# Kernel optimization log

Measured on AMD Instinct MI355X. Metric: run time of the kernel, lower is better.

Reference implementation:

```python
import jax, jax.numpy as jnp
import numpy as np

H = 2048
MAX_DEPTH = 2
BASIS = 4


def setup_inputs() -> dict:
    key = jax.random.key(0)
    ks = jax.random.split(key, 16)
    s = 0.02

    def w(k, shape):
        return jax.random.normal(k, shape, dtype=jnp.float32) * s

    return dict(
        x=jax.random.normal(ks[0], (1, H), dtype=jnp.float32),
        h=jax.random.normal(ks[1], (1, H), dtype=jnp.float32),
        c=jax.random.normal(ks[2], (1, H), dtype=jnp.float32),
        Wq=w(ks[3], (H, H)), Wk=w(ks[4], (H, H)), Wv=w(ks[5], (H, H)), Wo=w(ks[6], (H, H)),
        Wih=w(ks[7], (H, 4 * H)), Whh=w(ks[8], (H, 4 * H)),
        b_lstm=jnp.zeros((4 * H,), jnp.float32),
        router_w=w(ks[9], (H, BASIS)), router_b=jnp.zeros((BASIS,), jnp.float32),
        expert_w=w(ks[10], (BASIS, H, H)), expert_b=jnp.zeros((BASIS, H), jnp.float32),
        dr_w=w(ks[11], (H, MAX_DEPTH + 1)),
        # bias the depth router toward the deepest choice so the recursion tree is exercised
        dr_b=jnp.array([0.0, 1.0, 5.0], jnp.float32),
        ram_w=w(ks[12], (2 * H, H)), ram_b=jnp.zeros((H,), jnp.float32),
        ag_w=w(ks[13], (2 * H, H)), ag_b=jnp.zeros((H,), jnp.float32),
    )


def reference(x, h, c, Wq, Wk, Wv, Wo, Wih, Whh, b_lstm, router_w, router_b,
              expert_w, expert_b, dr_w, dr_b, ram_w, ram_b, ag_w, ag_b):
    def cell_step(x_, h_, c_):
        # Single-token multi-head attention: softmax over a length-1 axis is
        # identically 1, so attention collapses to (h @ Wv) @ Wo; Wq/Wk are
        # parameters with zero effective gradient (matches torch behavior).
        attn = (h_ @ Wv) @ Wo
        gates = x_ @ Wih + attn @ Whh + b_lstm  # [1, 4H]
        i, f, g, o = jnp.split(gates, 4, axis=1)
        c2 = jax.nn.sigmoid(f) * c_ + jax.nn.sigmoid(i) * jnp.tanh(g)
        h2 = jax.nn.sigmoid(o) * jnp.tanh(c2)
        return h2, h2, c2

    def path_gate(hh):
        p = jax.nn.softmax(hh @ router_w + router_b, axis=1)          # [1, E]
        eo = jnp.einsum('bh,ehk->bek', hh, expert_w) + expert_b        # [1, E, H]
        return jnp.einsum('be,bek->bk', p, eo)                         # [1, H]

    def ramanujan(states):
        # alternating-harmonic (Ramanujan-summation style) weighted reduction
        agg = states[0] * 0.0
        for n, s in enumerate(states):
            agg = agg + (((-1.0) ** n) / (n + 1)) * s
        return jnp.concatenate([agg, states[0]], axis=1) @ ram_w + ram_b

    def fwd(x_, h_, c_, depth):
        so, hs, cs = cell_step(x_, h_, c_)
        hp = path_gate(hs)
        # mirrors torch.no_grad() + .item() host sync
        chosen = int(jnp.argmax(hp @ dr_w + dr_b, axis=1)[0])
        steps = min(chosen, max(0, MAX_DEPTH - depth))
        if steps <= 0:
            return so, hp, cs
        h_cur, c_cur, final = hp, cs, so
        states = [h_cur]
        for _ in range(steps):
            damping = 1.0 / (depth + 1) ** 2
            ro, hnr, cn = fwd(x_, h_cur, c_cur, depth + 1)
            h_next = h_cur + damping * (hnr - h_cur)  # torch.lerp
            states.append(h_next)
            h_cur, c_cur, final = h_next, cn, ro
        anchor = ramanujan(states)
        g = jax.nn.sigmoid(jnp.concatenate([h_cur, anchor], axis=1) @ ag_w + ag_b)
        return final, g * anchor + (1.0 - g) * h_cur, c_cur

    return fwd(x, h, c, 0)
```

## Files before the change

kernel.cpp:

```cpp
#include <hip/hip_runtime.h>
#include <math.h>


#define H 2048
#define NB 512
#define PREP_NB 2048
typedef unsigned short u16;
typedef float f4v __attribute__((ext_vector_type(4)));

struct P {
  const float *x, *h0, *c0, *Wv, *Wo, *Wih, *Whh, *b_lstm, *router_w, *router_b,
              *expert_w, *expert_b, *dr_w, *dr_b, *ram_w, *ram_b, *ag_w, *ag_b;
  const u16 *bWv, *bWo, *bWhh, *bEx;
  float* out;
  float* ws;
};

constexpr int CTRU   = 8192;
constexpr int DL     = 8192;
constexpr int GT     = 8208;
constexpr int NODE   = 16400;
constexpr int NODESZ = 26624;
constexpr int THV = 0, ATT = 2048, GAC = 4096, EO = 12288, SO = 20480, CS = 22528, HP = 24576;
constexpr int FIN    = NODE + 5 * NODESZ;
constexpr int FINSZ  = 8192;
constexpr int ANC = 0, GCC = 2048, HNo = 4096, AGGo = 6144;
constexpr int RH1 = FIN + 3 * FINSZ;
constexpr int RF1 = RH1 + 2048;
constexpr int RC1 = RH1 + 4096;
constexpr int ZTOT = 5 * 20480 + 3 * 4096;
constexpr size_t BF_BYTE_OFF = 786432;
constexpr size_t oWo  = 4194304;
constexpr size_t oWhh = 8388608;
constexpr size_t oEx  = 25165824;
constexpr size_t BF_TOT = 41943040;

__device__ __forceinline__ float sigm(float v) { return 1.f / (1.f + expf(-v)); }

__device__ __forceinline__ float coh_f(const float* p) {
  return __hip_atomic_load(p, __ATOMIC_RELAXED, __HIP_MEMORY_SCOPE_AGENT);
}
__device__ __forceinline__ void coh_st(float* p, float v) {
  __hip_atomic_store(p, v, __ATOMIC_RELAXED, __HIP_MEMORY_SCOPE_AGENT);
}

__device__ __forceinline__ float bfl(unsigned u) { union { unsigned x; float f; } c; c.x = u << 16; return c.f; }
__device__ __forceinline__ float bfh(unsigned u) { union { unsigned x; float f; } c; c.x = u & 0xFFFF0000u; return c.f; }
__device__ __forceinline__ u16 f2bf(float f) {
  unsigned u = __float_as_uint(f);
  u += 0x7FFFu + ((u >> 16) & 1u);
  return (u16)(u >> 16);
}

template <typename WT> struct W4;
template <> struct W4<float> {
  static __device__ __forceinline__ void load(const float* p, float* w) {
    const float4 v = *reinterpret_cast<const float4*>(p);
    w[0] = v.x; w[1] = v.y; w[2] = v.z; w[3] = v.w;
  }
};
template <> struct W4<u16> {
  static __device__ __forceinline__ void load(const u16* p, float* w) {
    const uint2 u = *reinterpret_cast<const uint2*>(p);
    w[0] = bfl(u.x); w[1] = bfh(u.x); w[2] = bfl(u.y); w[3] = bfh(u.y);
  }
};

template <typename WT> __device__ __forceinline__ const WT* selWv(const P& p);
template <> __device__ __forceinline__ const float* selWv<float>(const P& p) { return p.Wv; }
template <> __device__ __forceinline__ const u16*   selWv<u16>(const P& p)   { return p.bWv; }
template <typename WT> __device__ __forceinline__ const WT* selWo(const P& p);
template <> __device__ __forceinline__ const float* selWo<float>(const P& p) { return p.Wo; }
template <> __device__ __forceinline__ const u16*   selWo<u16>(const P& p)   { return p.bWo; }
template <typename WT> __device__ __forceinline__ const WT* selWhh(const P& p);
template <> __device__ __forceinline__ const float* selWhh<float>(const P& p) { return p.Whh; }
template <> __device__ __forceinline__ const u16*   selWhh<u16>(const P& p)   { return p.bWhh; }
template <typename WT> __device__ __forceinline__ const WT* selEx(const P& p);
template <> __device__ __forceinline__ const float* selEx<float>(const P& p) { return p.expert_w; }
template <> __device__ __forceinline__ const u16*   selEx<u16>(const P& p)   { return p.bEx; }

__device__ __forceinline__ int dsteps(const float* dla, const float* drb, int mx) {
  const float l0 = dla[0] + drb[0], l1 = dla[1] + drb[1], l2 = dla[2] + drb[2];
  int ch = 0; float bv = l0;
  if (l1 > bv) { bv = l1; ch = 1; }
  if (l2 > bv) { bv = l2; ch = 2; }
  return ch < mx ? ch : mx;
}

__device__ __forceinline__ bool pred(const float* ws, const float* drb, int code) {
  if (code == 0) return true;
  const int s0 = dsteps(ws + DL, drb, 2);
  switch (code) {
    case 1: return s0 >= 1;
    case 2: return s0 >= 1 && dsteps(ws + DL + 4, drb, 1) >= 1;
    case 3: return s0 >= 2;
    case 4: return s0 >= 2 && dsteps(ws + DL + 8, drb, 1) >= 1;
  }
  return true;
}

__device__ __forceinline__ void resbar(unsigned* ctr, int phase) {
  asm volatile("s_waitcnt vmcnt(0)" ::: "memory");
  __syncthreads();
  __shared__ int lastB;
  if (threadIdx.x == 0) {
    lastB = 0;
    unsigned* line = ctr + (blockIdx.x & 31) * 16;
    const unsigned prev = __hip_atomic_fetch_add(line, 1u, __ATOMIC_RELAXED, __HIP_MEMORY_SCOPE_AGENT);
    if (prev == (unsigned)(16 * phase) - 1u) {
      const unsigned m = __hip_atomic_fetch_add(ctr + 32 * 16, 1u, __ATOMIC_RELAXED, __HIP_MEMORY_SCOPE_AGENT);
      if (m == (unsigned)(32 * phase) - 1u) lastB = 1;
    }
  }
  __syncthreads();
  if (lastB) {
    if (threadIdx.x < 32)
      __hip_atomic_store(ctr + (33 + threadIdx.x) * 16, (unsigned)phase,
                         __ATOMIC_RELAXED, __HIP_MEMORY_SCOPE_AGENT);
  } else if (threadIdx.x == 0) {
    const unsigned* rel = ctr + (33 + (blockIdx.x & 31)) * 16;
    long t = 0;
    while (__hip_atomic_load(rel, __ATOMIC_RELAXED, __HIP_MEMORY_SCOPE_AGENT) < (unsigned)phase) {
      __builtin_amdgcn_s_sleep(2);
      if (++t > 30000000L) break;
    }
  }
  __syncthreads();
}

template <int CHUNK, int XMODE, typename WT>
__device__ __forceinline__ void gemv_phase(
    int bid, int G,
    const float* xA, const float* xB, int splitPt, const float* xBias,
    const WT* __restrict__ W, float* __restrict__ y, int N,
    float* shx, float4* red)
{
  const int tid = threadIdx.x, lane = tid & 63, tsub = tid >> 6;
  const int g = bid % G, s = bid / G;
  const int base = s * CHUNK;
  for (int idx = tid; idx < CHUNK; idx += 256) {
    const int i = base + idx;
    float v;
    if (XMODE == 0)      v = (i < splitPt) ? xA[i] : xB[i - splitPt];
    else if (XMODE == 1) v = coh_f(xA + i);
    else                 v = (i < splitPt) ? xA[i] : (xBias[i - splitPt] + coh_f(xB + (i - splitPt)));
    shx[idx] = v;
  }
  __syncthreads();
  constexpr int LEN = CHUNK / 4;
  const int j = (g << 8) + (lane << 2);
  const WT* Wp = W + (size_t)(base + tsub * LEN) * N + j;
  float ax = 0.f, ay = 0.f, az = 0.f, aw = 0.f;
#pragma unroll
  for (int t = 0; t < LEN; ++t) {
    const float xi = shx[tsub * LEN + t];
    float w[4];
    W4<WT>::load(Wp + (size_t)t * N, w);
    ax = fmaf(xi, w[0], ax); ay = fmaf(xi, w[1], ay);
    az = fmaf(xi, w[2], az); aw = fmaf(xi, w[3], aw);
  }
  red[tid] = make_float4(ax, ay, az, aw);
  __syncthreads();
  if (tsub == 0) {
    float4 a = red[tid], b = red[tid + 64], c = red[tid + 128], d = red[tid + 192];
    atomicAdd(&y[j + 0], a.x + b.x + c.x + d.x);
    atomicAdd(&y[j + 1], a.y + b.y + c.y + d.y);
    atomicAdd(&y[j + 2], a.z + b.z + c.z + d.z);
    atomicAdd(&y[j + 3], a.w + b.w + c.w + d.w);
  }
}

template <typename WT>
__device__ void expert_phase(const P& p, float* nb, const float* c_in, const float* gt,
                             float* shx, float4* red)
{
  const int tid = threadIdx.x, lane = tid & 63, w = tid >> 6;
  const int g = blockIdx.x & 31, s = blockIdx.x >> 5;
  const int i0 = s * 128;
  if (tid < 128) {
    const int i = i0 + tid;
    const float gi = p.b_lstm[i]         + coh_f(gt + i)         + coh_f(nb + GAC + i);
    const float gf = p.b_lstm[H + i]     + coh_f(gt + H + i)     + coh_f(nb + GAC + H + i);
    const float gg = p.b_lstm[2 * H + i] + coh_f(gt + 2 * H + i) + coh_f(nb + GAC + 2 * H + i);
    const float go = p.b_lstm[3 * H + i] + coh_f(gt + 3 * H + i) + coh_f(nb + GAC + 3 * H + i);
    const float c2 = sigm(gf) * c_in[i] + sigm(gi) * tanhf(gg);
    const float h2 = sigm(go) * tanhf(c2);
    shx[tid] = h2;
    if (g == 0) { coh_st(nb + SO + i, h2); coh_st(nb + CS + i, c2); }
  }
  __syncthreads();
  const int j = (g << 8) + (lane << 2);
  const int e = j >> 11, k = j & (H - 1);
  const WT* Wp = selEx<WT>(p) + ((size_t)e << 22) + (size_t)(i0 + w * 32) * H + k;
  float ax = 0.f, ay = 0.f, az = 0.f, aw = 0.f;
#pragma unroll
  for (int t = 0; t < 32; ++t) {
    const float xi = shx[w * 32 + t];
    float wv[4];
    W4<WT>::load(Wp + (size_t)t * H, wv);
    ax = fmaf(xi, wv[0], ax); ay = fmaf(xi, wv[1], ay);
    az = fmaf(xi, wv[2], az); aw = fmaf(xi, wv[3], aw);
  }
  red[tid] = make_float4(ax, ay, az, aw);
  __syncthreads();
  if (w == 0) {
    float4 a = red[tid], b = red[tid + 64], c = red[tid + 128], d = red[tid + 192];
    atomicAdd(&nb[EO + j + 0], a.x + b.x + c.x + d.x);
    atomicAdd(&nb[EO + j + 1], a.y + b.y + c.y + d.y);
    atomicAdd(&nb[EO + j + 2], a.z + b.z + c.z + d.z);
    atomicAdd(&nb[EO + j + 3], a.w + b.w + c.w + d.w);
  }
}

__device__ void combine_phase(const P& p, float* nb, float* dla, int leaf, float damping,
                              const float* php, float* hn, float* agg, float4* red)
{
  const int tid = threadIdx.x;
  float r0 = 0.f, r1 = 0.f, r2 = 0.f, r3 = 0.f;
  for (int i = tid; i < H; i += 256) {
    const float hh = coh_f(nb + SO + i);
    const float4 rw = *reinterpret_cast<const float4*>(p.router_w + i * 4);
    r0 = fmaf(hh, rw.x, r0); r1 = fmaf(hh, rw.y, r1);
    r2 = fmaf(hh, rw.z, r2); r3 = fmaf(hh, rw.w, r3);
  }
  red[tid] = make_float4(r0, r1, r2, r3);
  __syncthreads();
  for (int off = 128; off > 0; off >>= 1) {
    if (tid < off) {
      const float4 b = red[tid + off];
      red[tid].x += b.x; red[tid].y += b.y; red[tid].z += b.z; red[tid].w += b.w;
    }
    __syncthreads();
  }
  const float4 L = red[0];
  __syncthreads();
  const float l0 = L.x + p.router_b[0], l1 = L.y + p.router_b[1];
  const float l2 = L.z + p.router_b[2], l3 = L.w + p.router_b[3];
  const float m = fmaxf(fmaxf(l0, l1), fmaxf(l2, l3));
  const float e0 = expf(l0 - m), e1 = expf(l1 - m), e2 = expf(l2 - m), e3 = expf(l3 - m);
  const float inv = 1.f / (e0 + e1 + e2 + e3);
  const float q0 = e0 * inv, q1 = e1 * inv, q2 = e2 * inv, q3 = e3 * inv;
  const int jj = blockIdx.x * 256 + tid;
  const float v = q0 * (p.expert_b[jj]         + coh_f(nb + EO + jj))
                + q1 * (p.expert_b[H + jj]     + coh_f(nb + EO + H + jj))
                + q2 * (p.expert_b[2 * H + jj] + coh_f(nb + EO + 2 * H + jj))
                + q3 * (p.expert_b[3 * H + jj] + coh_f(nb + EO + 3 * H + jj));
  if (leaf) {
    const float h0v = php[jj];
    const float hnv = h0v + damping * (v - h0v);
    hn[jj] = hnv;
    agg[jj] = h0v - 0.5f * hnv;
  } else {
    nb[HP + jj] = v;
    red[tid] = make_float4(v * p.dr_w[jj * 3 + 0], v * p.dr_w[jj * 3 + 1], v * p.dr_w[jj * 3 + 2], 0.f);
    __syncthreads();
    for (int off = 128; off > 0; off >>= 1) {
      if (tid < off) {
        const float4 b = red[tid + off];
        red[tid].x += b.x; red[tid].y += b.y; red[tid].z += b.z;
      }
      __syncthreads();
    }
    if (tid == 0) {
      atomicAdd(&dla[0], red[0].x);
      atomicAdd(&dla[1], red[0].y);
      atomicAdd(&dla[2], red[0].z);
    }
  }
}

__device__ void tail_fsel(const P& p, float* ws) {
  if (dsteps(ws + DL, p.dr_b, 2) < 1) return;
  const bool deep = dsteps(ws + DL + 4, p.dr_b, 1) >= 1;
  const int jj = blockIdx.x * 256 + threadIdx.x;
  const float* n1 = ws + NODE + 1 * NODESZ;
  const float* n2 = ws + NODE + 2 * NODESZ;
  const float* fb = ws + FIN;
  float rh, rf, rc;
  if (deep) {
    const float gacc = p.ag_b[jj] + coh_f(fb + GCC + jj);
    const float anc  = p.ram_b[jj] + coh_f(fb + ANC + jj);
    const float g = sigm(gacc);
    rh = g * anc + (1.f - g) * fb[HNo + jj];
    rf = n2[SO + jj]; rc = n2[CS + jj];
  } else {
    rh = n1[HP + jj]; rf = n1[SO + jj]; rc = n1[CS + jj];
  }
  ws[RH1 + jj] = rh; ws[RF1 + jj] = rf; ws[RC1 + jj] = rc;
}

__device__ void tail1(const P& p, float* ws) {
  const int s0 = dsteps(ws + DL, p.dr_b, 2);
  if (s0 < 1) return;
  const int jj = blockIdx.x * 256 + threadIdx.x;
  const float* n0 = ws + NODE;
  const float* n3 = ws + NODE + 3 * NODESZ;
  const float* n4 = ws + NODE + 4 * NODESZ;
  const float* fb3 = ws + FIN + FINSZ;
  float* fb0 = ws + FIN + 2 * FINSZ;
  const float r1 = ws[RH1 + jj];
  float rh3 = 0.f, rf3 = 0.f, rc3 = 0.f;
  if (s0 >= 2) {
    if (dsteps(ws + DL + 8, p.dr_b, 1) >= 1) {
      const float gacc = p.ag_b[jj] + coh_f(fb3 + GCC + jj);
      const float anc  = p.ram_b[jj] + coh_f(fb3 + ANC + jj);
      const float g = sigm(gacc);
      rh3 = g * anc + (1.f - g) * fb3[HNo + jj];
      rf3 = n4[SO + jj]; rc3 = n4[CS + jj];
    } else { rh3 = n3[HP + jj]; rf3 = n3[SO + jj]; rc3 = n3[CS + jj]; }
  }
  float ag = n0[HP + jj] - 0.5f * r1;
  float hc, oF, oC;
  if (s0 >= 2) { ag += (1.f / 3.f) * rh3; hc = rh3; oF = rf3; oC = rc3; }
  else { hc = r1; oF = ws[RF1 + jj]; oC = ws[RC1 + jj]; }
  fb0[AGGo + jj] = ag; fb0[HNo + jj] = hc;
  p.out[jj] = oF; p.out[2 * H + jj] = oC;
}

__device__ void tail2(const P& p, float* ws) {
  const int s0 = dsteps(ws + DL, p.dr_b, 2);
  const int jj = blockIdx.x * 256 + threadIdx.x;
  const float* n0 = ws + NODE;
  const float* fb0 = ws + FIN + 2 * FINSZ;
  if (s0 == 0) {
    p.out[jj] = n0[SO + jj]; p.out[H + jj] = n0[HP + jj]; p.out[2 * H + jj] = n0[CS + jj];
  } else {
    const float gacc = p.ag_b[jj] + coh_f(fb0 + GCC + jj);
    const float anc  = p.ram_b[jj] + coh_f(fb0 + ANC + jj);
    const float g = sigm(gacc);
    p.out[H + jj] = g * anc + (1.f - g) * fb0[HNo + jj];
  }
}

__global__ void __launch_bounds__(256) k_zero(P p) {
  float* ws = p.ws;
  const int gtid = blockIdx.x * 256 + threadIdx.x;
  const int gsz = gridDim.x * 256;
  unsigned* u = (unsigned*)ws;
  for (int i = gtid; i < CTRU; i += gsz) u[i] = 0u;
  if (gtid < 12) ws[DL + gtid] = 0.f;
  for (int i = gtid; i < 8192; i += gsz) ws[GT + i] = 0.f;
}

__global__ void __launch_bounds__(256) k_prep(P p, u16* bf, int doConv) {
  float* ws = p.ws;
  __shared__ float shx[128];
  __shared__ float4 red[256];
  const size_t gtid = (size_t)blockIdx.x * 256 + threadIdx.x;
  const size_t nthr = (size_t)PREP_NB * 256;
  for (size_t i = gtid; i < (size_t)ZTOT; i += nthr) {
    if (i < 5 * 20480) {
      const int n = (int)(i / 20480), off = (int)(i % 20480);
      ws[NODE + n * NODESZ + off] = 0.f;
    } else {
      const int j = (int)(i - 5 * 20480);
      ws[FIN + (j >> 12) * FINSZ + (j & 4095)] = 0.f;
    }
  }
  if (doConv) {
    auto conv = [&](const float* __restrict__ src, u16* __restrict__ dst, size_t elems) {
      for (size_t c = gtid; c < elems / 8; c += nthr) {
        const size_t e = c * 8;
        const f4v a = __builtin_nontemporal_load(reinterpret_cast<const f4v*>(src + e));
        const f4v b = __builtin_nontemporal_load(reinterpret_cast<const f4v*>(src + e + 4));
        uint4 o;
        o.x = (unsigned)f2bf(a.x) | ((unsigned)f2bf(a.y) << 16);
        o.y = (unsigned)f2bf(a.z) | ((unsigned)f2bf(a.w) << 16);
        o.z = (unsigned)f2bf(b.x) | ((unsigned)f2bf(b.y) << 16);
        o.w = (unsigned)f2bf(b.z) | ((unsigned)f2bf(b.w) << 16);
        *reinterpret_cast<uint4*>(dst + e) = o;
      }
    };
    conv(p.Wv,       bf,         oWo);
    conv(p.Wo,       bf + oWo,   oWhh - oWo);
    conv(p.Whh,      bf + oWhh,  oEx - oWhh);
    conv(p.expert_w, bf + oEx,   BF_TOT - oEx);
  }
  gemv_phase<32, 0, float>(blockIdx.x, 32, p.x, p.x, 1 << 30, nullptr,
                           p.Wih, ws + GT, 4 * H, shx, red);
}

template <typename WT>
__global__ void __launch_bounds__(256, 2) k_node(
    P p, int nodeIdx, int ctrIdx, int predCode,
    const float* hv, const float* cv,
    int leaf, float damping, const float* php, float* hn, float* agg, float* dla)
{
  float* ws = p.ws;
  if (!pred(ws, p.dr_b, predCode)) return;
  __shared__ float shx[128];
  __shared__ float4 red[256];
  float* nb = ws + NODE + nodeIdx * NODESZ;
  unsigned* ctr = (unsigned*)ws + ctrIdx * 1024;
  gemv_phase<32, 0, WT>(blockIdx.x, 8, hv, hv, 1 << 30, nullptr, selWv<WT>(p), nb + THV, H, shx, red);
  resbar(ctr, 1);
  gemv_phase<32, 1, WT>(blockIdx.x, 8, nb + THV, nullptr, 0, nullptr, selWo<WT>(p), nb + ATT, H, shx, red);
  resbar(ctr, 2);
  gemv_phase<128, 1, WT>(blockIdx.x, 32, nb + ATT, nullptr, 0, nullptr, selWhh<WT>(p), nb + GAC, 4 * H, shx, red);
  resbar(ctr, 3);
  expert_phase<WT>(p, nb, cv, ws + GT, shx, red);
  resbar(ctr, 4);
  if (blockIdx.x >= 8) return;
  combine_phase(p, nb, dla, leaf, damping, php, hn, agg, red);
}

__global__ void __launch_bounds__(256, 2) k_fin(
    P p, int finIdx, int ctrIdx, int predCode,
    const float* aggv, const float* phpv, const float* hnv, int tailKind)
{
  float* ws = p.ws;
  __shared__ float shx[64];
  __shared__ float4 red[256];
  float* fb = ws + FIN + finIdx * FINSZ;
  unsigned* ctr = (unsigned*)ws + ctrIdx * 1024;
  const bool ok = pred(ws, p.dr_b, predCode);
  if (ok) {
    gemv_phase<64, 0, float>(blockIdx.x, 8, aggv, phpv, H, nullptr, p.ram_w, fb + ANC, H, shx, red);
    resbar(ctr, 1);
    gemv_phase<64, 2, float>(blockIdx.x, 8, hnv, fb + ANC, H, p.ram_b, p.ag_w, fb + GCC, H, shx, red);
    resbar(ctr, 2);
  }
  if (blockIdx.x >= 8) return;
  if (tailKind == 1) tail_fsel(p, ws);
  else if (tailKind == 2) tail1(p, ws);
  else tail2(p, ws);
}

extern "C" void kernel_launch(void* const* d_in, const int* in_sizes, int n_in,
                              void* d_out, int out_size, void* d_ws, size_t ws_size,
                              hipStream_t stream) {
  P p;
  p.x = (const float*)d_in[0];  p.h0 = (const float*)d_in[1];  p.c0 = (const float*)d_in[2];
  p.Wv = (const float*)d_in[5]; p.Wo = (const float*)d_in[6];
  p.Wih = (const float*)d_in[7]; p.Whh = (const float*)d_in[8];
  p.b_lstm = (const float*)d_in[9];
  p.router_w = (const float*)d_in[10]; p.router_b = (const float*)d_in[11];
  p.expert_w = (const float*)d_in[12]; p.expert_b = (const float*)d_in[13];
  p.dr_w = (const float*)d_in[14]; p.dr_b = (const float*)d_in[15];
  p.ram_w = (const float*)d_in[16]; p.ram_b = (const float*)d_in[17];
  p.ag_w = (const float*)d_in[18]; p.ag_b = (const float*)d_in[19];
  p.out = (float*)d_out;
  p.ws = (float*)d_ws;

  const bool useBf = ws_size >= BF_BYTE_OFF + BF_TOT * 2 + 1024;
  u16* bf = (u16*)((char*)d_ws + BF_BYTE_OFF);
  p.bWv  = bf;
  p.bWo  = bf + oWo;
  p.bWhh = bf + oWhh;
  p.bEx  = bf + oEx;

  float* ws = p.ws;
  auto nb = [&](int n) { return ws + NODE + n * NODESZ; };
  float* fb1 = ws + FIN;
  float* fb3 = ws + FIN + FINSZ;
  float* fb0 = ws + FIN + 2 * FINSZ;

  auto node = [&](int n, int ctrIdx, int predCode, const float* hv, const float* cv,
                  int leaf, float damping, const float* php, float* hn, float* agg, float* dla) {
    if (useBf)
      k_node<u16><<<NB, 256, 0, stream>>>(p, n, ctrIdx, predCode, hv, cv, leaf, damping, php, hn, agg, dla);
    else
      k_node<float><<<NB, 256, 0, stream>>>(p, n, ctrIdx, predCode, hv, cv, leaf, damping, php, hn, agg, dla);
  };

  k_zero<<<16, 256, 0, stream>>>(p);
  k_prep<<<PREP_NB, 256, 0, stream>>>(p, bf, useBf ? 1 : 0);
  node(0, 0, 0, p.h0, p.c0, 0, 0.f, nullptr, nullptr, nullptr, ws + DL);
  node(1, 1, 1, nb(0) + HP, nb(0) + CS, 0, 0.f, nullptr, nullptr, nullptr, ws + DL + 4);
  node(2, 2, 2, nb(1) + HP, nb(1) + CS, 1, 0.25f, nb(1) + HP, fb1 + HNo, fb1 + AGGo, nullptr);
  k_fin<<<NB, 256, 0, stream>>>(p, 0, 3, 2, fb1 + AGGo, nb(1) + HP, fb1 + HNo, 1);
  node(3, 4, 3, ws + RH1, ws + RC1, 0, 0.f, nullptr, nullptr, nullptr, ws + DL + 8);
  node(4, 5, 4, nb(3) + HP, nb(3) + CS, 1, 0.25f, nb(3) + HP, fb3 + HNo, fb3 + AGGo, nullptr);
  k_fin<<<NB, 256, 0, stream>>>(p, 1, 6, 4, fb3 + AGGo, nb(3) + HP, fb3 + HNo, 2);
  k_fin<<<NB, 256, 0, stream>>>(p, 2, 7, 1, fb0 + AGGo, nb(0) + HP, fb0 + HNo, 3);
}
```

Baseline: 357.2 us.

## Fuse recursion-tree node and finalize kernels into one persistent megakernel

```diff
diff --git a/kernel.cpp b/kernel.cpp
--- a/kernel.cpp
+++ b/kernel.cpp
@@ -79,24 +79,14 @@
 template <> __device__ __forceinline__ const float* selEx<float>(const P& p) { return p.expert_w; }
 template <> __device__ __forceinline__ const u16*   selEx<u16>(const P& p)   { return p.bEx; }
 
-__device__ __forceinline__ int dsteps(const float* dla, const float* drb, int mx) {
-  const float l0 = dla[0] + drb[0], l1 = dla[1] + drb[1], l2 = dla[2] + drb[2];
+__device__ __forceinline__ int dstepsC(const float* dla, const float* drb, int mx) {
+  const float l0 = coh_f(dla + 0) + drb[0];
+  const float l1 = coh_f(dla + 1) + drb[1];
+  const float l2 = coh_f(dla + 2) + drb[2];
   int ch = 0; float bv = l0;
   if (l1 > bv) { bv = l1; ch = 1; }
   if (l2 > bv) { bv = l2; ch = 2; }
   return ch < mx ? ch : mx;
-}
-
-__device__ __forceinline__ bool pred(const float* ws, const float* drb, int code) {
-  if (code == 0) return true;
-  const int s0 = dsteps(ws + DL, drb, 2);
-  switch (code) {
-    case 1: return s0 >= 1;
-    case 2: return s0 >= 1 && dsteps(ws + DL + 4, drb, 1) >= 1;
-    case 3: return s0 >= 2;
-    case 4: return s0 >= 2 && dsteps(ws + DL + 8, drb, 1) >= 1;
-  }
-  return true;
 }
 
 __device__ __forceinline__ void resbar(unsigned* ctr, int phase) {
@@ -108,17 +98,17 @@
     unsigned* line = ctr + (blockIdx.x & 31) * 16;
     const unsigned prev = __hip_atomic_fetch_add(line, 1u, __ATOMIC_RELAXED, __HIP_MEMORY_SCOPE_AGENT);
     if (prev == (unsigned)(16 * phase) - 1u) {
-      const unsigned m = __hip_atomic_fetch_add(ctr + 32 * 16, 1u, __ATOMIC_RELAXED, __HIP_MEMORY_SCOPE_AGENT);
+      const unsigned m = __hip_atomic_fetch_add(ctr + 512, 1u, __ATOMIC_RELAXED, __HIP_MEMORY_SCOPE_AGENT);
       if (m == (unsigned)(32 * phase) - 1u) lastB = 1;
     }
   }
   __syncthreads();
   if (lastB) {
     if (threadIdx.x < 32)
-      __hip_atomic_store(ctr + (33 + threadIdx.x) * 16, (unsigned)phase,
+      __hip_atomic_store(ctr + (40 + threadIdx.x) * 16, (unsigned)phase,
                          __ATOMIC_RELAXED, __HIP_MEMORY_SCOPE_AGENT);
   } else if (threadIdx.x == 0) {
-    const unsigned* rel = ctr + (33 + (blockIdx.x & 31)) * 16;
+    const unsigned* rel = ctr + (40 + (blockIdx.x & 31)) * 16;
     long t = 0;
     while (__hip_atomic_load(rel, __ATOMIC_RELAXED, __HIP_MEMORY_SCOPE_AGENT) < (unsigned)phase) {
       __builtin_amdgcn_s_sleep(2);
@@ -141,9 +131,10 @@
   for (int idx = tid; idx < CHUNK; idx += 256) {
     const int i = base + idx;
     float v;
-    if (XMODE == 0)      v = (i < splitPt) ? xA[i] : xB[i - splitPt];
+    if (XMODE == 0)      v = (i < splitPt) ? coh_f(xA + i) : coh_f(xB + (i - splitPt));
     else if (XMODE == 1) v = coh_f(xA + i);
-    else                 v = (i < splitPt) ? xA[i] : (xBias[i - splitPt] + coh_f(xB + (i - splitPt)));
+    else                 v = (i < splitPt) ? coh_f(xA + i)
+                                           : (xBias[i - splitPt] + coh_f(xB + (i - splitPt)));
     shx[idx] = v;
   }
   __syncthreads();
@@ -168,6 +159,7 @@
     atomicAdd(&y[j + 2], a.z + b.z + c.z + d.z);
     atomicAdd(&y[j + 3], a.w + b.w + c.w + d.w);
   }
+  __syncthreads();
 }
 
 template <typename WT>
@@ -183,7 +175,7 @@
     const float gf = p.b_lstm[H + i]     + coh_f(gt + H + i)     + coh_f(nb + GAC + H + i);
     const float gg = p.b_lstm[2 * H + i] + coh_f(gt + 2 * H + i) + coh_f(nb + GAC + 2 * H + i);
     const float go = p.b_lstm[3 * H + i] + coh_f(gt + 3 * H + i) + coh_f(nb + GAC + 3 * H + i);
-    const float c2 = sigm(gf) * c_in[i] + sigm(gi) * tanhf(gg);
+    const float c2 = sigm(gf) * coh_f(c_in + i) + sigm(gi) * tanhf(gg);
     const float h2 = sigm(go) * tanhf(c2);
     shx[tid] = h2;
     if (g == 0) { coh_st(nb + SO + i, h2); coh_st(nb + CS + i, c2); }
@@ -210,6 +202,7 @@
     atomicAdd(&nb[EO + j + 2], a.z + b.z + c.z + d.z);
     atomicAdd(&nb[EO + j + 3], a.w + b.w + c.w + d.w);
   }
+  __syncthreads();
 }
 
 __device__ void combine_phase(const P& p, float* nb, float* dla, int leaf, float damping,
@@ -240,18 +233,18 @@
   const float e0 = expf(l0 - m), e1 = expf(l1 - m), e2 = expf(l2 - m), e3 = expf(l3 - m);
   const float inv = 1.f / (e0 + e1 + e2 + e3);
   const float q0 = e0 * inv, q1 = e1 * inv, q2 = e2 * inv, q3 = e3 * inv;
-  const int jj = blockIdx.x * 256 + tid;
+  const int jj = (int)blockIdx.x * 256 + tid;
   const float v = q0 * (p.expert_b[jj]         + coh_f(nb + EO + jj))
                 + q1 * (p.expert_b[H + jj]     + coh_f(nb + EO + H + jj))
                 + q2 * (p.expert_b[2 * H + jj] + coh_f(nb + EO + 2 * H + jj))
                 + q3 * (p.expert_b[3 * H + jj] + coh_f(nb + EO + 3 * H + jj));
   if (leaf) {
-    const float h0v = php[jj];
+    const float h0v = coh_f(php + jj);
     const float hnv = h0v + damping * (v - h0v);
-    hn[jj] = hnv;
-    agg[jj] = h0v - 0.5f * hnv;
+    coh_st(hn + jj, hnv);
+    coh_st(agg + jj, h0v - 0.5f * hnv);
   } else {
-    nb[HP + jj] = v;
+    coh_st(nb + HP + jj, v);
     red[tid] = make_float4(v * p.dr_w[jj * 3 + 0], v * p.dr_w[jj * 3 + 1], v * p.dr_w[jj * 3 + 2], 0.f);
     __syncthreads();
     for (int off = 128; off > 0; off >>= 1) {
@@ -269,10 +262,8 @@
   }
 }
 
-__device__ void tail_fsel(const P& p, float* ws) {
-  if (dsteps(ws + DL, p.dr_b, 2) < 1) return;
-  const bool deep = dsteps(ws + DL + 4, p.dr_b, 1) >= 1;
-  const int jj = blockIdx.x * 256 + threadIdx.x;
+__device__ void tail_fsel(const P& p, float* ws, bool deep) {
+  const int jj = (int)blockIdx.x * 256 + threadIdx.x;
   const float* n1 = ws + NODE + 1 * NODESZ;
   const float* n2 = ws + NODE + 2 * NODESZ;
   const float* fb = ws + FIN;
@@ -281,54 +272,55 @@
     const float gacc = p.ag_b[jj] + coh_f(fb + GCC + jj);
     const float anc  = p.ram_b[jj] + coh_f(fb + ANC + jj);
     const float g = sigm(gacc);
-    rh = g * anc + (1.f - g) * fb[HNo + jj];
-    rf = n2[SO + jj]; rc = n2[CS + jj];
+    rh = g * anc + (1.f - g) * coh_f(fb + HNo + jj);
+    rf = coh_f(n2 + SO + jj); rc = coh_f(n2 + CS + jj);
   } else {
-    rh = n1[HP + jj]; rf = n1[SO + jj]; rc = n1[CS + jj];
-  }
-  ws[RH1 + jj] = rh; ws[RF1 + jj] = rf; ws[RC1 + jj] = rc;
-}
-
-__device__ void tail1(const P& p, float* ws) {
-  const int s0 = dsteps(ws + DL, p.dr_b, 2);
-  if (s0 < 1) return;
-  const int jj = blockIdx.x * 256 + threadIdx.x;
+    rh = coh_f(n1 + HP + jj); rf = coh_f(n1 + SO + jj); rc = coh_f(n1 + CS + jj);
+  }
+  coh_st(ws + RH1 + jj, rh); coh_st(ws + RF1 + jj, rf); coh_st(ws + RC1 + jj, rc);
+}
+
+__device__ void tail1(const P& p, float* ws, int s0, bool deep3) {
+  const int jj = (int)blockIdx.x * 256 + threadIdx.x;
   const float* n0 = ws + NODE;
   const float* n3 = ws + NODE + 3 * NODESZ;
   const float* n4 = ws + NODE + 4 * NODESZ;
   const float* fb3 = ws + FIN + FINSZ;
   float* fb0 = ws + FIN + 2 * FINSZ;
-  const float r1 = ws[RH1 + jj];
+  const float r1 = coh_f(ws + RH1 + jj);
   float rh3 = 0.f, rf3 = 0.f, rc3 = 0.f;
   if (s0 >= 2) {
-    if (dsteps(ws + DL + 8, p.dr_b, 1) >= 1) {
+    if (deep3) {
       const float gacc = p.ag_b[jj] + coh_f(fb3 + GCC + jj);
       const float anc  = p.ram_b[jj] + coh_f(fb3 + ANC + jj);
       const float g = sigm(gacc);
-      rh3 = g * anc + (1.f - g) * fb3[HNo + jj];
-      rf3 = n4[SO + jj]; rc3 = n4[CS + jj];
-    } else { rh3 = n3[HP + jj]; rf3 = n3[SO + jj]; rc3 = n3[CS + jj]; }
-  }
-  float ag = n0[HP + jj] - 0.5f * r1;
+      rh3 = g * anc + (1.f - g) * coh_f(fb3 + HNo + jj);
+      rf3 = coh_f(n4 + SO + jj); rc3 = coh_f(n4 + CS + jj);
+    } else {
+      rh3 = coh_f(n3 + HP + jj); rf3 = coh_f(n3 + SO + jj); rc3 = coh_f(n3 + CS + jj);
+    }
+  }
+  float ag = coh_f(n0 + HP + jj) - 0.5f * r1;
   float hc, oF, oC;
   if (s0 >= 2) { ag += (1.f / 3.f) * rh3; hc = rh3; oF = rf3; oC = rc3; }
-  else { hc = r1; oF = ws[RF1 + jj]; oC = ws[RC1 + jj]; }
-  fb0[AGGo + jj] = ag; fb0[HNo + jj] = hc;
+  else { hc = r1; oF = coh_f(ws + RF1 + jj); oC = coh_f(ws + RC1 + jj); }
+  coh_st(fb0 + AGGo + jj, ag); coh_st(fb0 + HNo + jj, hc);
   p.out[jj] = oF; p.out[2 * H + jj] = oC;
 }
 
-__device__ void tail2(const P& p, float* ws) {
-  const int s0 = dsteps(ws + DL, p.dr_b, 2);
-  const int jj = blockIdx.x * 256 + threadIdx.x;
+__device__ void tail2(const P& p, float* ws, int s0) {
+  const int jj = (int)blockIdx.x * 256 + threadIdx.x;
   const float* n0 = ws + NODE;
   const float* fb0 = ws + FIN + 2 * FINSZ;
   if (s0 == 0) {
-    p.out[jj] = n0[SO + jj]; p.out[H + jj] = n0[HP + jj]; p.out[2 * H + jj] = n0[CS + jj];
+    p.out[jj] = coh_f(n0 + SO + jj);
+    p.out[H + jj] = coh_f(n0 + HP + jj);
+    p.out[2 * H + jj] = coh_f(n0 + CS + jj);
   } else {
     const float gacc = p.ag_b[jj] + coh_f(fb0 + GCC + jj);
     const float anc  = p.ram_b[jj] + coh_f(fb0 + ANC + jj);
     const float g = sigm(gacc);
-    p.out[H + jj] = g * anc + (1.f - g) * fb0[HNo + jj];
+    p.out[H + jj] = g * anc + (1.f - g) * coh_f(fb0 + HNo + jj);
   }
 }
 
@@ -344,7 +336,7 @@
 
 __global__ void __launch_bounds__(256) k_prep(P p, u16* bf, int doConv) {
   float* ws = p.ws;
-  __shared__ float shx[128];
+  __shared__ float shx[256];
   __shared__ float4 red[256];
   const size_t gtid = (size_t)blockIdx.x * 256 + threadIdx.x;
   const size_t nthr = (size_t)PREP_NB * 256;
@@ -381,49 +373,72 @@
 }
 
 template <typename WT>
-__global__ void __launch_bounds__(256, 2) k_node(
-    P p, int nodeIdx, int ctrIdx, int predCode,
-    const float* hv, const float* cv,
-    int leaf, float damping, const float* php, float* hn, float* agg, float* dla)
-{
+__global__ void __launch_bounds__(256, 2) k_mega(P p) {
   float* ws = p.ws;
-  if (!pred(ws, p.dr_b, predCode)) return;
-  __shared__ float shx[128];
+  __shared__ float shx[256];
   __shared__ float4 red[256];
-  float* nb = ws + NODE + nodeIdx * NODESZ;
-  unsigned* ctr = (unsigned*)ws + ctrIdx * 1024;
-  gemv_phase<32, 0, WT>(blockIdx.x, 8, hv, hv, 1 << 30, nullptr, selWv<WT>(p), nb + THV, H, shx, red);
-  resbar(ctr, 1);
-  gemv_phase<32, 1, WT>(blockIdx.x, 8, nb + THV, nullptr, 0, nullptr, selWo<WT>(p), nb + ATT, H, shx, red);
-  resbar(ctr, 2);
-  gemv_phase<128, 1, WT>(blockIdx.x, 32, nb + ATT, nullptr, 0, nullptr, selWhh<WT>(p), nb + GAC, 4 * H, shx, red);
-  resbar(ctr, 3);
-  expert_phase<WT>(p, nb, cv, ws + GT, shx, red);
-  resbar(ctr, 4);
-  if (blockIdx.x >= 8) return;
-  combine_phase(p, nb, dla, leaf, damping, php, hn, agg, red);
-}
-
-__global__ void __launch_bounds__(256, 2) k_fin(
-    P p, int finIdx, int ctrIdx, int predCode,
-    const float* aggv, const float* phpv, const float* hnv, int tailKind)
-{
-  float* ws = p.ws;
-  __shared__ float shx[64];
-  __shared__ float4 red[256];
-  float* fb = ws + FIN + finIdx * FINSZ;
-  unsigned* ctr = (unsigned*)ws + ctrIdx * 1024;
-  const bool ok = pred(ws, p.dr_b, predCode);
-  if (ok) {
+  unsigned* ctr = (unsigned*)ws;
+  int ph = 0;
+  float* fb1 = ws + FIN;
+  float* fb3 = ws + FIN + FINSZ;
+  float* fb0 = ws + FIN + 2 * FINSZ;
+
+  auto node_sec = [&](int nodeIdx, const float* hv, const float* cv,
+                      int leaf, float damping, const float* php, float* hn, float* agg,
+                      float* dla) {
+    float* nb = ws + NODE + nodeIdx * NODESZ;
+    gemv_phase<32, 1, WT>(blockIdx.x, 8, hv, nullptr, 0, nullptr, selWv<WT>(p), nb + THV, H, shx, red);
+    resbar(ctr, ++ph);
+    gemv_phase<32, 1, WT>(blockIdx.x, 8, nb + THV, nullptr, 0, nullptr, selWo<WT>(p), nb + ATT, H, shx, red);
+    resbar(ctr, ++ph);
+    gemv_phase<128, 1, WT>(blockIdx.x, 32, nb + ATT, nullptr, 0, nullptr, selWhh<WT>(p), nb + GAC, 4 * H, shx, red);
+    resbar(ctr, ++ph);
+    expert_phase<WT>(p, nb, cv, ws + GT, shx, red);
+    resbar(ctr, ++ph);
+    if (blockIdx.x < 8)
+      combine_phase(p, nb, dla, leaf, damping, php, hn, agg, red);
+    resbar(ctr, ++ph);
+  };
+  auto fin_gemvs = [&](float* fb, const float* aggv, const float* phpv, const float* hnv) {
     gemv_phase<64, 0, float>(blockIdx.x, 8, aggv, phpv, H, nullptr, p.ram_w, fb + ANC, H, shx, red);
-    resbar(ctr, 1);
+    resbar(ctr, ++ph);
     gemv_phase<64, 2, float>(blockIdx.x, 8, hnv, fb + ANC, H, p.ram_b, p.ag_w, fb + GCC, H, shx, red);
-    resbar(ctr, 2);
-  }
-  if (blockIdx.x >= 8) return;
-  if (tailKind == 1) tail_fsel(p, ws);
-  else if (tailKind == 2) tail1(p, ws);
-  else tail2(p, ws);
+    resbar(ctr, ++ph);
+  };
+
+  node_sec(0, p.h0, p.c0, 0, 0.f, nullptr, nullptr, nullptr, ws + DL);
+  const int s0 = dstepsC(ws + DL, p.dr_b, 2);
+
+  if (s0 >= 1) {
+    float* n0 = ws + NODE;
+    float* n1 = ws + NODE + NODESZ;
+    float* n3 = ws + NODE + 3 * NODESZ;
+    node_sec(1, n0 + HP, n0 + CS, 0, 0.f, nullptr, nullptr, nullptr, ws + DL + 4);
+    const int s1 = dstepsC(ws + DL + 4, p.dr_b, 1);
+    if (s1 >= 1) {
+      node_sec(2, n1 + HP, n1 + CS, 1, 0.25f, n1 + HP, fb1 + HNo, fb1 + AGGo, nullptr);
+      fin_gemvs(fb1, fb1 + AGGo, n1 + HP, fb1 + HNo);
+    }
+    if (blockIdx.x < 8) tail_fsel(p, ws, s1 >= 1);
+    resbar(ctr, ++ph);
+
+    int s3 = 0;
+    if (s0 >= 2) {
+      node_sec(3, ws + RH1, ws + RC1, 0, 0.f, nullptr, nullptr, nullptr, ws + DL + 8);
+      s3 = dstepsC(ws + DL + 8, p.dr_b, 1);
+      if (s3 >= 1) {
+        node_sec(4, n3 + HP, n3 + CS, 1, 0.25f, n3 + HP, fb3 + HNo, fb3 + AGGo, nullptr);
+        fin_gemvs(fb3, fb3 + AGGo, n3 + HP, fb3 + HNo);
+      }
+    }
+    if (blockIdx.x < 8) tail1(p, ws, s0, s3 >= 1);
+    resbar(ctr, ++ph);
+
+    fin_gemvs(fb0, fb0 + AGGo, n0 + HP, fb0 + HNo);
+    if (blockIdx.x < 8) tail2(p, ws, s0);
+  } else {
+    if (blockIdx.x < 8) tail2(p, ws, 0);
+  }
 }
 
 extern "C" void kernel_launch(void* const* d_in, const int* in_sizes, int n_in,
@@ -449,28 +464,10 @@
   p.bWhh = bf + oWhh;
   p.bEx  = bf + oEx;
 
-  float* ws = p.ws;
-  auto nb = [&](int n) { return ws + NODE + n * NODESZ; };
-  float* fb1 = ws + FIN;
-  float* fb3 = ws + FIN + FINSZ;
-  float* fb0 = ws + FIN + 2 * FINSZ;
-
-  auto node = [&](int n, int ctrIdx, int predCode, const float* hv, const float* cv,
-                  int leaf, float damping, const float* php, float* hn, float* agg, float* dla) {
-    if (useBf)
-      k_node<u16><<<NB, 256, 0, stream>>>(p, n, ctrIdx, predCode, hv, cv, leaf, damping, php, hn, agg, dla);
-    else
-      k_node<float><<<NB, 256, 0, stream>>>(p, n, ctrIdx, predCode, hv, cv, leaf, damping, php, hn, agg, dla);
-  };
-
   k_zero<<<16, 256, 0, stream>>>(p);
   k_prep<<<PREP_NB, 256, 0, stream>>>(p, bf, useBf ? 1 : 0);
-  node(0, 0, 0, p.h0, p.c0, 0, 0.f, nullptr, nullptr, nullptr, ws + DL);
-  node(1, 1, 1, nb(0) + HP, nb(0) + CS, 0, 0.f, nullptr, nullptr, nullptr, ws + DL + 4);
-  node(2, 2, 2, nb(1) + HP, nb(1) + CS, 1, 0.25f, nb(1) + HP, fb1 + HNo, fb1 + AGGo, nullptr);
-  k_fin<<<NB, 256, 0, stream>>>(p, 0, 3, 2, fb1 + AGGo, nb(1) + HP, fb1 + HNo, 1);
-  node(3, 4, 3, ws + RH1, ws + RC1, 0, 0.f, nullptr, nullptr, nullptr, ws + DL + 8);
-  node(4, 5, 4, nb(3) + HP, nb(3) + CS, 1, 0.25f, nb(3) + HP, fb3 + HNo, fb3 + AGGo, nullptr);
-  k_fin<<<NB, 256, 0, stream>>>(p, 1, 6, 4, fb3 + AGGo, nb(3) + HP, fb3 + HNo, 2);
-  k_fin<<<NB, 256, 0, stream>>>(p, 2, 7, 1, fb0 + AGGo, nb(0) + HP, fb0 + HNo, 3);
-}
+  if (useBf)
+    k_mega<u16><<<NB, 256, 0, stream>>>(p);
+  else
+    k_mega<float><<<NB, 256, 0, stream>>>(p);
+}
```

After: 366.4 us. 2.6% more time.
